# Kernel tuning notes

Measured on AMD Instinct MI355X. Metric: run time of the kernel, lower is better.

The kernel has to match this reference:

```python
import jax, jax.numpy as jnp
import numpy as np

EPSILON = 1e-06
N_TOKENS = 65536
WIDTH_IN = 1024
WIDTH_OUT = 1024
NUM_HEAD = 16
DIM_HEAD = 64


def setup_inputs() -> dict:
    key = jax.random.key(0)
    k_x, k_b, k_lin, k_ker = jax.random.split(key, 4)
    x = jax.random.normal(k_x, (N_TOKENS, WIDTH_IN), dtype=jnp.float32)
    norm_bias = jax.random.normal(k_b, (N_TOKENS, NUM_HEAD, DIM_HEAD), dtype=jnp.float32)
    # LinearLayer: std = 1/sqrt(width_in), shape (width_in, num_head*dim_head)
    w_lin = jax.random.normal(k_lin, (WIDTH_IN, NUM_HEAD * DIM_HEAD), dtype=jnp.float32) / np.sqrt(WIDTH_IN)
    # Grouped kernel: (num_head, dim_head, width_out // num_head), scaled 1/sqrt(dim_head)
    kernel = jax.random.normal(k_ker, (NUM_HEAD, DIM_HEAD, WIDTH_OUT // NUM_HEAD), dtype=jnp.float32) / np.sqrt(DIM_HEAD)
    return {"x": x, "norm_bias": norm_bias, "w_lin": w_lin, "kernel": kernel}


def reference(x, norm_bias, w_lin, kernel):
    # Dense projection, bias-free
    xx = x @ w_lin                                   # [N, H*D]
    xx = xx.reshape(*x.shape[:-1], NUM_HEAD, DIM_HEAD)  # [N, H, D]
    # Per-head RMSNorm
    xx = xx / jnp.sqrt(jnp.mean(jnp.square(xx), axis=-1, keepdims=True) + EPSILON)
    # Optional norm-bias blend
    xx = (xx + norm_bias.reshape(xx.shape)) / 2 ** 0.5
    # Per-head grouped matmul
    xx = jnp.einsum('nhd,hdf->nhf', xx, kernel)      # [N, H, F]
    return xx.reshape(*x.shape[:-1], -1)             # [N, H*F]
```

## Files before the change

kernel.cpp:

```cpp
#include <hip/hip_runtime.h>


typedef __attribute__((ext_vector_type(8))) __bf16 bf16x8;
typedef __attribute__((ext_vector_type(4))) float f32x4;
typedef __attribute__((ext_vector_type(8))) unsigned short ushort8;

__device__ __forceinline__ unsigned short bfbits(float f) {
  return __builtin_bit_cast(unsigned short, (__bf16)f);
}
__device__ __forceinline__ f32x4 mfma_bf16(bf16x8 a, bf16x8 b, f32x4 c) {
  return __builtin_amdgcn_mfma_f32_16x16x32_bf16(a, b, c, 0, 0, 0);
}
__device__ __forceinline__ void gl_lds16(const void* g, void* l) {
  __builtin_amdgcn_global_load_lds(
      (const __attribute__((address_space(1))) unsigned int*)g,
      (__attribute__((address_space(3))) unsigned int*)l, 16, 0, 0);
}

__global__ void cvt_x(const float* __restrict__ x, unsigned short* __restrict__ xb, int n8) {
  int i = blockIdx.x * blockDim.x + threadIdx.x;
  const int stride = gridDim.x * blockDim.x;
  for (; i < n8; i += stride) {
    f32x4 a = *reinterpret_cast<const f32x4*>(x + (size_t)i * 8);
    f32x4 b = *reinterpret_cast<const f32x4*>(x + (size_t)i * 8 + 4);
    ushort8 v;
    v[0] = bfbits(a[0]); v[1] = bfbits(a[1]); v[2] = bfbits(a[2]); v[3] = bfbits(a[3]);
    v[4] = bfbits(b[0]); v[5] = bfbits(b[1]); v[6] = bfbits(b[2]); v[7] = bfbits(b[3]);
    *reinterpret_cast<ushort8*>(xb + (size_t)i * 8) = v;
  }
}

__global__ void prep_w2(const float* __restrict__ w, unsigned short* __restrict__ wb) {
  const int t = blockIdx.x, ct = blockIdx.y, col = threadIdx.x;
  #pragma unroll
  for (int kc = 0; kc < 4; ++kc) {
    ushort8 v;
    #pragma unroll
    for (int j = 0; j < 8; ++j)
      v[j] = bfbits(w[(size_t)(t * 32 + kc * 8 + j) * 1024 + ct * 128 + col]);
    *reinterpret_cast<ushort8*>(wb + (((size_t)(ct * 32 + t) * 4 + kc) * 128 + col) * 8) = v;
  }
}

__global__ void transpose_k(const float* __restrict__ kin, unsigned short* __restrict__ kt) {
  __shared__ float tile[64][65];
  const int h = blockIdx.x;
  const int t = threadIdx.x;
  #pragma unroll
  for (int i = 0; i < 16; ++i) {
    int idx = i * 256 + t;
    tile[idx >> 6][idx & 63] = kin[(size_t)h * 4096 + idx];
  }
  __syncthreads();
  #pragma unroll
  for (int i = 0; i < 16; ++i) {
    int idx = i * 256 + t;
    kt[(size_t)h * 4096 + idx] = bfbits(tile[idx & 63][idx >> 6]);
  }
}

__global__ __launch_bounds__(256, 4)
void fused_main(const unsigned short* __restrict__ xb,
                const float* __restrict__ nbias,
                const unsigned short* __restrict__ wb,
                const unsigned short* __restrict__ ktg,
                float* __restrict__ out)
{
  __shared__ __align__(16) unsigned char smem[32768];
  const int tid = threadIdx.x;
  const int wv = tid >> 6, lane = tid & 63, l15 = lane & 15, lg = lane >> 4;
  const int wr = wv >> 1, wc = wv & 1;
  const int bid = blockIdx.x;
  const int gx = bid & 7, slot = bid >> 3;
  const int v = gx * 512 + slot;
  const int rt = v >> 3, ct = v & 7;
  const size_t row0 = (size_t)rt * 128;

  const unsigned char* xrow = reinterpret_cast<const unsigned char*>(xb) + row0 * 2048;
  const unsigned char* wsrc = reinterpret_cast<const unsigned char*>(wb) + (size_t)ct * 262144;

  const int c0 = tid,       r0_ = c0 >> 2, s0_ = c0 & 3;
  const int c1 = 256 + tid, r1_ = c1 >> 2;
  const unsigned char* asrc0 = xrow + r0_ * 2048 + ((s0_ ^ ((r0_ >> 1) & 3)) << 4);
  const unsigned char* asrc1 = xrow + r1_ * 2048 + ((s0_ ^ ((r1_ >> 1) & 3)) << 4);

  const int swz_a = (l15 >> 1) & 3;
  const int abase = (wr * 64 + l15) * 64 + ((lg ^ swz_a) << 4);
  const int bbase = lg * 2048 + (wc * 64 + l15) * 16;

  f32x4 acc[4][4];
  const f32x4 z4 = {0.f, 0.f, 0.f, 0.f};
  #pragma unroll
  for (int mi = 0; mi < 4; ++mi)
    #pragma unroll
    for (int ni = 0; ni < 4; ++ni) acc[mi][ni] = z4;

  auto stageA = [&](int t, int bsel) {
    unsigned char* Ab = smem + (bsel << 13);
    gl_lds16(asrc0 + (size_t)t * 64, Ab + tid * 16);
    gl_lds16(asrc1 + (size_t)t * 64, Ab + 4096 + tid * 16);
  };
  auto stageB = [&](int t, int bsel) {
    unsigned char* Bb = smem + 16384 + (bsel << 13);
    const unsigned char* bs = wsrc + (size_t)t * 8192;
    gl_lds16(bs + tid * 16,        Bb + tid * 16);
    gl_lds16(bs + 4096 + tid * 16, Bb + 4096 + tid * 16);
  };
  auto compute = [&](int csel) {
    const unsigned char* Ab = smem + (csel << 13);
    const unsigned char* Bb = smem + 16384 + (csel << 13);
    bf16x8 af[4], bq[4];
    #pragma unroll
    for (int mi = 0; mi < 4; ++mi)
      af[mi] = *reinterpret_cast<const bf16x8*>(Ab + abase + mi * 1024);
    #pragma unroll
    for (int ni = 0; ni < 4; ++ni)
      bq[ni] = *reinterpret_cast<const bf16x8*>(Bb + bbase + ni * 256);
    __builtin_amdgcn_s_setprio(1);
    #pragma unroll
    for (int mi = 0; mi < 4; ++mi)
      #pragma unroll
      for (int ni = 0; ni < 4; ++ni)
        acc[mi][ni] = mfma_bf16(af[mi], bq[ni], acc[mi][ni]);
    __builtin_amdgcn_s_setprio(0);
  };

  stageA(0, 0);
  stageB(0, 0);

  for (int t = 0; t < 32; ++t) {
    __syncthreads();
    const int cur = t & 1, nxt = cur ^ 1;
    if (t + 1 < 32) { stageA(t + 1, nxt); stageB(t + 1, nxt); }
    compute(cur);
  }
  __syncthreads();

  const int h = ct * 2 + wc;
  unsigned short* yw = reinterpret_cast<unsigned short*>(smem) + wv * 4096;
  const float* bb = nbias + (row0 + wr * 64) * 1024 + (size_t)h * 64 + l15;

  #pragma unroll
  for (int mi = 0; mi < 4; ++mi) {
    float ss[4];
    #pragma unroll
    for (int r = 0; r < 4; ++r) {
      float p = 0.f;
      #pragma unroll
      for (int ni = 0; ni < 4; ++ni) { const float q = acc[mi][ni][r]; p += q * q; }
      ss[r] = p;
    }
    #pragma unroll
    for (int s = 1; s < 16; s <<= 1)
      #pragma unroll
      for (int r = 0; r < 4; ++r) ss[r] += __shfl_xor(ss[r], s, 64);
    #pragma unroll
    for (int r = 0; r < 4; ++r) {
      const float rs = rsqrtf(ss[r] * 0.015625f + 1e-6f);
      const int rl = mi * 16 + lg * 4 + r;
      const float* bp = bb + (size_t)rl * 1024;
      #pragma unroll
      for (int ni = 0; ni < 4; ++ni) {
        const float y = (acc[mi][ni][r] * rs + bp[ni * 16]) * 0.70710678118654752f;
        yw[rl * 64 + ((ni * 16 + l15) ^ ((rl & 7) << 3))] = bfbits(y);
      }
    }
  }

  const unsigned short* ktp = ktg + (size_t)h * 4096;
  bf16x8 b2[4][2];
  #pragma unroll
  for (int ff = 0; ff < 4; ++ff)
    #pragma unroll
    for (int ks = 0; ks < 2; ++ks)
      b2[ff][ks] = *reinterpret_cast<const bf16x8*>(ktp + (ff * 16 + l15) * 64 + ks * 32 + lg * 8);

  #pragma unroll
  for (int m2 = 0; m2 < 4; ++m2) {
    f32x4 a2[4] = {z4, z4, z4, z4};
    const int row = m2 * 16 + l15;
    #pragma unroll
    for (int ks = 0; ks < 2; ++ks) {
      bf16x8 a = *reinterpret_cast<const bf16x8*>(
          yw + row * 64 + ((ks * 32 + lg * 8) ^ ((row & 7) << 3)));
      #pragma unroll
      for (int ff = 0; ff < 4; ++ff) a2[ff] = mfma_bf16(a, b2[ff][ks], a2[ff]);
    }
    float* ob = out + (row0 + wr * 64 + m2 * 16 + lg * 4) * 1024 + ct * 128 + wc * 64 + l15;
    #pragma unroll
    for (int ff = 0; ff < 4; ++ff)
      #pragma unroll
      for (int r = 0; r < 4; ++r)
        ob[(size_t)r * 1024 + ff * 16] = a2[ff][r];
  }
}

extern "C" void kernel_launch(void* const* d_in, const int* in_sizes, int n_in,
                              void* d_out, int out_size, void* d_ws, size_t ws_size,
                              hipStream_t stream) {
  const float* x  = (const float*)d_in[0];
  const float* nb = (const float*)d_in[1];
  const float* wl = (const float*)d_in[2];
  const float* kr = (const float*)d_in[3];
  float* out = (float*)d_out;

  unsigned short* wbp = (unsigned short*)d_ws;
  unsigned short* ktp = wbp + 1048576;
  unsigned short* xbp = (unsigned short*)((char*)d_ws + 2228224);

  hipLaunchKernelGGL(prep_w2, dim3(32, 8), dim3(128), 0, stream, wl, wbp);
  hipLaunchKernelGGL(transpose_k, dim3(16), dim3(256), 0, stream, kr, ktp);
  hipLaunchKernelGGL(cvt_x, dim3(2048), dim3(256), 0, stream, x, xbp, 65536 * 128);
  hipLaunchKernelGGL(fused_main, dim3(4096), dim3(256), 0, stream, xbp, nb, wbp, ktp, out);
}
```

Before: 321.4 us.

## Enlarge GEMM tile to 256x256 with 8 waves and phased LDS pipeline

Grows the fused kernel's output tile from 128x128 to 256x256 with 512 threads and a 64-wide K step, using 128KB of LDS in double buffers. The weight prep kernel is rewritten to emit a swizzled layout that matches the new LDS reads. Each K step is split into four MFMA phases separated by barriers, with the next A and B stages issued between phases. The aim is more data reuse per byte loaded and better overlap of loads with MFMA work. The cost is lower occupancy, more barriers and heavy register pressure from the 8x4 accumulator array.

```diff
diff --git a/kernel.cpp b/kernel.cpp
--- a/kernel.cpp
+++ b/kernel.cpp
@@ -30,15 +30,19 @@
   }
 }
 
-__global__ void prep_w2(const float* __restrict__ w, unsigned short* __restrict__ wb) {
-  const int t = blockIdx.x, ct = blockIdx.y, col = threadIdx.x;
-  #pragma unroll
-  for (int kc = 0; kc < 4; ++kc) {
+__global__ void prep_w(const float* __restrict__ w, unsigned short* __restrict__ wb) {
+  const int img = blockIdx.x;
+  const int ct = img >> 5, ktg = (img >> 1) & 15, half = img & 1;
+  #pragma unroll
+  for (int i = 0; i < 4; ++i) {
+    const int q = i * 256 + threadIdx.x;
+    const int c = q >> 3, s = q & 7;
+    const int k0 = ktg * 64 + 8 * (s ^ (c & 7));
+    const int col = ct * 256 + half * 128 + c;
     ushort8 v;
     #pragma unroll
-    for (int j = 0; j < 8; ++j)
-      v[j] = bfbits(w[(size_t)(t * 32 + kc * 8 + j) * 1024 + ct * 128 + col]);
-    *reinterpret_cast<ushort8*>(wb + (((size_t)(ct * 32 + t) * 4 + kc) * 128 + col) * 8) = v;
+    for (int j = 0; j < 8; ++j) v[j] = bfbits(w[(size_t)(k0 + j) * 1024 + col]);
+    *reinterpret_cast<ushort8*>(wb + (size_t)img * 8192 + (size_t)q * 8) = v;
   }
 }
 
@@ -59,115 +63,175 @@
   }
 }
 
-__global__ __launch_bounds__(256, 4)
+__global__ __launch_bounds__(512, 2)
 void fused_main(const unsigned short* __restrict__ xb,
                 const float* __restrict__ nbias,
                 const unsigned short* __restrict__ wb,
-                const unsigned short* __restrict__ ktg,
+                const unsigned short* __restrict__ ktg_,
                 float* __restrict__ out)
 {
-  __shared__ __align__(16) unsigned char smem[32768];
+  __shared__ __align__(16) unsigned char smem[131072];
   const int tid = threadIdx.x;
   const int wv = tid >> 6, lane = tid & 63, l15 = lane & 15, lg = lane >> 4;
-  const int wr = wv >> 1, wc = wv & 1;
+  const int l7 = l15 & 7;
+  const int wr = wv >> 2, wc = wv & 3;
   const int bid = blockIdx.x;
-  const int gx = bid & 7, slot = bid >> 3;
-  const int v = gx * 512 + slot;
-  const int rt = v >> 3, ct = v & 7;
-  const size_t row0 = (size_t)rt * 128;
-
-  const unsigned char* xrow = reinterpret_cast<const unsigned char*>(xb) + row0 * 2048;
-  const unsigned char* wsrc = reinterpret_cast<const unsigned char*>(wb) + (size_t)ct * 262144;
-
-  const int c0 = tid,       r0_ = c0 >> 2, s0_ = c0 & 3;
-  const int c1 = 256 + tid, r1_ = c1 >> 2;
-  const unsigned char* asrc0 = xrow + r0_ * 2048 + ((s0_ ^ ((r0_ >> 1) & 3)) << 4);
-  const unsigned char* asrc1 = xrow + r1_ * 2048 + ((s0_ ^ ((r1_ >> 1) & 3)) << 4);
-
-  const int swz_a = (l15 >> 1) & 3;
-  const int abase = (wr * 64 + l15) * 64 + ((lg ^ swz_a) << 4);
-  const int bbase = lg * 2048 + (wc * 64 + l15) * 16;
-
-  f32x4 acc[4][4];
+  const int v = (bid & 7) * 128 + (bid >> 3);
+  const int rt = v >> 2, ct = v & 3;
+  const size_t row0 = (size_t)rt * 256;
+
+  const char* xB = (const char*)xb;
+  const char* wB = (const char*)wb + (size_t)ct * 524288;
+
+  const int su = tid >> 3, ss = tid & 7;
+  const char* asrc = xB + (row0 + su) * 2048 + ((ss ^ (su & 7)) << 4);
+
+  const int aO0 = wr * 16384 + l15 * 128 + ((lg ^ l7) << 4);
+  const int aO1 = wr * 16384 + l15 * 128 + (((4 + lg) ^ l7) << 4);
+  const int bH  = 65536 + (wc >> 1) * 16384 + ((wc & 1) * 64 + l15) * 128;
+  const int bO0 = bH + ((lg ^ l7) << 4);
+  const int bO1 = bH + (((4 + lg) ^ l7) << 4);
+
+  f32x4 acc[8][4];
   const f32x4 z4 = {0.f, 0.f, 0.f, 0.f};
   #pragma unroll
-  for (int mi = 0; mi < 4; ++mi)
+  for (int mi = 0; mi < 8; ++mi)
     #pragma unroll
     for (int ni = 0; ni < 4; ++ni) acc[mi][ni] = z4;
 
-  auto stageA = [&](int t, int bsel) {
-    unsigned char* Ab = smem + (bsel << 13);
-    gl_lds16(asrc0 + (size_t)t * 64, Ab + tid * 16);
-    gl_lds16(asrc1 + (size_t)t * 64, Ab + 4096 + tid * 16);
+  auto stageA2 = [&](int kt, int buf) {
+    unsigned char* d = smem + (buf << 15) + tid * 16;
+    const char* s0 = asrc + (size_t)kt * 128;
+    gl_lds16(s0,          d);
+    gl_lds16(s0 + 131072, d + 8192);
+    gl_lds16(s0 + 262144, d + 16384);
+    gl_lds16(s0 + 393216, d + 24576);
   };
-  auto stageB = [&](int t, int bsel) {
-    unsigned char* Bb = smem + 16384 + (bsel << 13);
-    const unsigned char* bs = wsrc + (size_t)t * 8192;
-    gl_lds16(bs + tid * 16,        Bb + tid * 16);
-    gl_lds16(bs + 4096 + tid * 16, Bb + 4096 + tid * 16);
+  auto stageB2 = [&](int kt, int buf) {
+    unsigned char* d = smem + 65536 + (buf << 15) + tid * 16;
+    const char* s0 = wB + (size_t)kt * 32768 + tid * 16;
+    gl_lds16(s0,         d);
+    gl_lds16(s0 + 8192,  d + 8192);
+    gl_lds16(s0 + 16384, d + 16384);
+    gl_lds16(s0 + 24576, d + 24576);
   };
-  auto compute = [&](int csel) {
-    const unsigned char* Ab = smem + (csel << 13);
-    const unsigned char* Bb = smem + 16384 + (csel << 13);
-    bf16x8 af[4], bq[4];
-    #pragma unroll
-    for (int mi = 0; mi < 4; ++mi)
-      af[mi] = *reinterpret_cast<const bf16x8*>(Ab + abase + mi * 1024);
-    #pragma unroll
-    for (int ni = 0; ni < 4; ++ni)
-      bq[ni] = *reinterpret_cast<const bf16x8*>(Bb + bbase + ni * 256);
-    __builtin_amdgcn_s_setprio(1);
-    #pragma unroll
-    for (int mi = 0; mi < 4; ++mi)
-      #pragma unroll
-      for (int ni = 0; ni < 4; ++ni)
-        acc[mi][ni] = mfma_bf16(af[mi], bq[ni], acc[mi][ni]);
-    __builtin_amdgcn_s_setprio(0);
-  };
-
-  stageA(0, 0);
-  stageB(0, 0);
-
-  for (int t = 0; t < 32; ++t) {
-    __syncthreads();
-    const int cur = t & 1, nxt = cur ^ 1;
-    if (t + 1 < 32) { stageA(t + 1, nxt); stageB(t + 1, nxt); }
-    compute(cur);
+
+  stageA2(0, 0);
+  stageB2(0, 0);
+  asm volatile("s_waitcnt vmcnt(0)" ::: "memory");
+  __builtin_amdgcn_s_barrier();
+
+  for (int tau = 0; tau < 16; ++tau) {
+    const int cb = tau & 1, nb = cb ^ 1;
+    const bool st = (tau + 1 < 16);
+    const unsigned char* S = smem + (cb << 15);
+    bf16x8 alo[4][2], ahi[4][2], blo[2][2], bhi[2][2];
+
+    #pragma unroll
+    for (int m = 0; m < 4; ++m) {
+      alo[m][0] = *reinterpret_cast<const bf16x8*>(S + aO0 + m * 2048);
+      alo[m][1] = *reinterpret_cast<const bf16x8*>(S + aO1 + m * 2048);
+    }
+    #pragma unroll
+    for (int n = 0; n < 2; ++n) {
+      blo[n][0] = *reinterpret_cast<const bf16x8*>(S + bO0 + n * 2048);
+      blo[n][1] = *reinterpret_cast<const bf16x8*>(S + bO1 + n * 2048);
+    }
+    if (st) stageA2(tau + 1, nb);
+    __builtin_amdgcn_s_barrier();
+    asm volatile("s_waitcnt lgkmcnt(0)" ::: "memory");
+    __builtin_amdgcn_s_setprio(1);
+    #pragma unroll
+    for (int m = 0; m < 4; ++m)
+      #pragma unroll
+      for (int n = 0; n < 2; ++n)
+        acc[m][n] = mfma_bf16(alo[m][1], blo[n][1],
+                    mfma_bf16(alo[m][0], blo[n][0], acc[m][n]));
+    __builtin_amdgcn_s_setprio(0);
+    __builtin_amdgcn_s_barrier();
+
+    #pragma unroll
+    for (int n = 0; n < 2; ++n) {
+      bhi[n][0] = *reinterpret_cast<const bf16x8*>(S + bO0 + (2 + n) * 2048);
+      bhi[n][1] = *reinterpret_cast<const bf16x8*>(S + bO1 + (2 + n) * 2048);
+    }
+    if (st) stageB2(tau + 1, nb);
+    __builtin_amdgcn_s_barrier();
+    asm volatile("s_waitcnt lgkmcnt(0)" ::: "memory");
+    __builtin_amdgcn_s_setprio(1);
+    #pragma unroll
+    for (int m = 0; m < 4; ++m)
+      #pragma unroll
+      for (int n = 0; n < 2; ++n)
+        acc[m][2 + n] = mfma_bf16(alo[m][1], bhi[n][1],
+                        mfma_bf16(alo[m][0], bhi[n][0], acc[m][2 + n]));
+    __builtin_amdgcn_s_setprio(0);
+    __builtin_amdgcn_s_barrier();
+
+    #pragma unroll
+    for (int m = 0; m < 4; ++m) {
+      ahi[m][0] = *reinterpret_cast<const bf16x8*>(S + aO0 + (4 + m) * 2048);
+      ahi[m][1] = *reinterpret_cast<const bf16x8*>(S + aO1 + (4 + m) * 2048);
+    }
+    __builtin_amdgcn_s_barrier();
+    asm volatile("s_waitcnt lgkmcnt(0)" ::: "memory");
+    __builtin_amdgcn_s_setprio(1);
+    #pragma unroll
+    for (int m = 0; m < 4; ++m)
+      #pragma unroll
+      for (int n = 0; n < 2; ++n)
+        acc[4 + m][n] = mfma_bf16(ahi[m][1], blo[n][1],
+                        mfma_bf16(ahi[m][0], blo[n][0], acc[4 + m][n]));
+    __builtin_amdgcn_s_setprio(0);
+    __builtin_amdgcn_s_barrier();
+
+    __builtin_amdgcn_s_setprio(1);
+    #pragma unroll
+    for (int m = 0; m < 4; ++m)
+      #pragma unroll
+      for (int n = 0; n < 2; ++n)
+        acc[4 + m][2 + n] = mfma_bf16(ahi[m][1], bhi[n][1],
+                            mfma_bf16(ahi[m][0], bhi[n][0], acc[4 + m][2 + n]));
+    __builtin_amdgcn_s_setprio(0);
+    if (st) asm volatile("s_waitcnt vmcnt(0)" ::: "memory");
+    __builtin_amdgcn_s_barrier();
   }
   __syncthreads();
 
-  const int h = ct * 2 + wc;
-  unsigned short* yw = reinterpret_cast<unsigned short*>(smem) + wv * 4096;
-  const float* bb = nbias + (row0 + wr * 64) * 1024 + (size_t)h * 64 + l15;
-
-  #pragma unroll
-  for (int mi = 0; mi < 4; ++mi) {
-    float ss[4];
+  const int h = ct * 4 + wc;
+  unsigned short* yw = reinterpret_cast<unsigned short*>(smem + wv * 16384);
+  const float* bb = nbias + (row0 + wr * 128) * 1024 + (size_t)h * 64 + l15;
+
+  #pragma unroll
+  for (int mi = 0; mi < 8; ++mi) {
+    float ssq[4];
     #pragma unroll
     for (int r = 0; r < 4; ++r) {
       float p = 0.f;
       #pragma unroll
       for (int ni = 0; ni < 4; ++ni) { const float q = acc[mi][ni][r]; p += q * q; }
-      ss[r] = p;
+      ssq[r] = p;
     }
     #pragma unroll
     for (int s = 1; s < 16; s <<= 1)
       #pragma unroll
-      for (int r = 0; r < 4; ++r) ss[r] += __shfl_xor(ss[r], s, 64);
+      for (int r = 0; r < 4; ++r) ssq[r] += __shfl_xor(ssq[r], s, 64);
     #pragma unroll
     for (int r = 0; r < 4; ++r) {
-      const float rs = rsqrtf(ss[r] * 0.015625f + 1e-6f);
+      const float rs = rsqrtf(ssq[r] * 0.015625f + 1e-6f);
       const int rl = mi * 16 + lg * 4 + r;
       const float* bp = bb + (size_t)rl * 1024;
       #pragma unroll
       for (int ni = 0; ni < 4; ++ni) {
         const float y = (acc[mi][ni][r] * rs + bp[ni * 16]) * 0.70710678118654752f;
-        yw[rl * 64 + ((ni * 16 + l15) ^ ((rl & 7) << 3))] = bfbits(y);
+        const int sy = (ni * 2 + (l15 >> 3)) ^ (rl & 7);
+        yw[rl * 64 + sy * 8 + l7] = bfbits(y);
       }
     }
   }
-
-  const unsigned short* ktp = ktg + (size_t)h * 4096;
+  asm volatile("s_waitcnt lgkmcnt(0)" ::: "memory");
+
+  const unsigned short* ktp = ktg_ + (size_t)h * 4096;
   bf16x8 b2[4][2];
   #pragma unroll
   for (int ff = 0; ff < 4; ++ff)
@@ -176,17 +240,17 @@
       b2[ff][ks] = *reinterpret_cast<const bf16x8*>(ktp + (ff * 16 + l15) * 64 + ks * 32 + lg * 8);
 
   #pragma unroll
-  for (int m2 = 0; m2 < 4; ++m2) {
+  for (int m2 = 0; m2 < 8; ++m2) {
     f32x4 a2[4] = {z4, z4, z4, z4};
     const int row = m2 * 16 + l15;
     #pragma unroll
     for (int ks = 0; ks < 2; ++ks) {
-      bf16x8 a = *reinterpret_cast<const bf16x8*>(
-          yw + row * 64 + ((ks * 32 + lg * 8) ^ ((row & 7) << 3)));
+      const int sl = ((ks * 4 + lg) ^ l7);
+      bf16x8 a = *reinterpret_cast<const bf16x8*>(yw + row * 64 + sl * 8);
       #pragma unroll
       for (int ff = 0; ff < 4; ++ff) a2[ff] = mfma_bf16(a, b2[ff][ks], a2[ff]);
     }
-    float* ob = out + (row0 + wr * 64 + m2 * 16 + lg * 4) * 1024 + ct * 128 + wc * 64 + l15;
+    float* ob = out + (row0 + wr * 128 + m2 * 16 + lg * 4) * 1024 + h * 64 + l15;
     #pragma unroll
     for (int ff = 0; ff < 4; ++ff)
       #pragma unroll
@@ -208,8 +272,8 @@
   unsigned short* ktp = wbp + 1048576;
   unsigned short* xbp = (unsigned short*)((char*)d_ws + 2228224);
 
-  hipLaunchKernelGGL(prep_w2, dim3(32, 8), dim3(128), 0, stream, wl, wbp);
+  hipLaunchKernelGGL(prep_w, dim3(128), dim3(256), 0, stream, wl, wbp);
   hipLaunchKernelGGL(transpose_k, dim3(16), dim3(256), 0, stream, kr, ktp);
   hipLaunchKernelGGL(cvt_x, dim3(2048), dim3(256), 0, stream, x, xbp, 65536 * 128);
-  hipLaunchKernelGGL(fused_main, dim3(4096), dim3(256), 0, stream, xbp, nb, wbp, ktp, out);
-}
+  hipLaunchKernelGGL(fused_main, dim3(1024), dim3(512), 0, stream, xbp, nb, wbp, ktp, out);
+}
```

Result: faster. 305.8 us (-4.9%).
